# Performance work log

Hardware: AMD Instinct MI355X
Metric: run time of the kernel (lower is better)

## Reference

```python
import jax, jax.numpy as jnp
import numpy as np

NEG_INF = -9e15
ALPHA = 0.2  # LeakyReLU negative slope


def setup_inputs() -> dict:
    key = jax.random.key(0)
    k1, k2, k3, k4 = jax.random.split(key, 4)
    B, N, C_IN, C_OUT, H = 8, 2048, 256, 256, 4
    node_feats = jax.random.normal(k1, (B, N, C_IN), dtype=jnp.float32)
    adj_matrix = jax.random.randint(k2, (B, N, N), 0, 2, dtype=jnp.int32)
    # include self-connections as the docstring expects
    eye = jnp.eye(N, dtype=jnp.int32)[None]
    adj_matrix = jnp.maximum(adj_matrix, eye)
    W = jax.random.normal(k3, (C_OUT, C_IN), dtype=jnp.float32) * (1.414 / np.sqrt(C_IN))
    b = jnp.zeros((C_OUT,), dtype=jnp.float32)
    a = jax.random.normal(k4, (H, 2 * (C_OUT // H)), dtype=jnp.float32) * 0.1
    return {"node_feats": node_feats, "adj_matrix": adj_matrix, "W": W, "b": b, "a": a}


def reference(node_feats, adj_matrix, W, b, a):
    B, N, _ = node_feats.shape
    H, two_c = a.shape
    c = two_c // 2
    # projection: [B, N, H, c]
    f = (jnp.einsum('bni,oi->bno', node_feats, W) + b).reshape(B, N, H, c)
    # attention logit for edge (i, j): leakyrelu(a . [f_i, f_j])
    # decomposes as leakyrelu(s_src[i] + s_dst[j])
    a_src, a_dst = a[:, :c], a[:, c:]
    s_src = jnp.einsum('bnhc,hc->bnh', f, a_src)  # [B, N, H]
    s_dst = jnp.einsum('bnhc,hc->bnh', f, a_dst)  # [B, N, H]
    logits = jax.nn.leaky_relu(s_src[:, :, None, :] + s_dst[:, None, :, :], ALPHA)  # [B,N,N,H]
    logits = jnp.where(adj_matrix[..., None] == 1, logits, NEG_INF)
    probs = jax.nn.softmax(logits, axis=2)  # softmax over source nodes j
    out = jnp.einsum('bijh,bjhc->bihc', probs, f)
    return out.reshape(B, N, H * c)  # concat_heads=True
```

## Files before the change

### kernel.cpp

```cpp
#include <hip/hip_runtime.h>

#define LOG2E 1.4426950408889634f

typedef __attribute__((ext_vector_type(8))) short short8;
typedef __attribute__((ext_vector_type(16))) float f32x16;

__device__ __forceinline__ unsigned short f2bf(float f) {
  unsigned int u = __float_as_uint(f);
  u = (u + 0x7fffu + ((u >> 16) & 1u)) >> 16;
  return (unsigned short)u;
}

__global__ __launch_bounds__(256) void gat_k1(
    const float* __restrict__ X, const float* __restrict__ W,
    const float* __restrict__ bias, const float* __restrict__ a,
    unsigned short* __restrict__ ft, float* __restrict__ ssrc,
    float* __restrict__ sdst)
{
  __shared__ float Xs[8][128];
  __shared__ float Ws[8][128];
  const int tid = threadIdx.x;
  const int tx = tid & 15, ty = tid >> 4;
  const int m0 = blockIdx.x * 128;
  const int c0 = blockIdx.y * 128;

  float acc[8][8];
#pragma unroll
  for (int r = 0; r < 8; ++r)
#pragma unroll
    for (int j = 0; j < 8; ++j) acc[r][j] = 0.f;

  const int lrow = tid >> 1;
  const int kk0 = (tid & 1) * 4;
  const float* Xp = X + (size_t)(m0 + lrow) * 256 + kk0;
  const float* Wp = W + (size_t)(c0 + lrow) * 256 + kk0;

  for (int kc = 0; kc < 256; kc += 8) {
    float4 xv = *(const float4*)(Xp + kc);
    float4 wv = *(const float4*)(Wp + kc);
    __syncthreads();
    Xs[kk0 + 0][lrow] = xv.x; Xs[kk0 + 1][lrow] = xv.y;
    Xs[kk0 + 2][lrow] = xv.z; Xs[kk0 + 3][lrow] = xv.w;
    Ws[kk0 + 0][lrow] = wv.x; Ws[kk0 + 1][lrow] = wv.y;
    Ws[kk0 + 2][lrow] = wv.z; Ws[kk0 + 3][lrow] = wv.w;
    __syncthreads();
#pragma unroll
    for (int kk = 0; kk < 8; ++kk) {
      float av[8], wv8[8];
#pragma unroll
      for (int r = 0; r < 8; ++r) av[r] = Xs[kk][ty * 8 + r];
#pragma unroll
      for (int j = 0; j < 8; ++j) wv8[j] = Ws[kk][tx * 8 + j];
#pragma unroll
      for (int r = 0; r < 8; ++r)
#pragma unroll
        for (int j = 0; j < 8; ++j) acc[r][j] = fmaf(av[r], wv8[j], acc[r][j]);
    }
  }

  const int b = m0 >> 11;
  const int nloc0 = (m0 & 2047) + ty * 8;
  const int cg0 = c0 + tx * 8;
  const int h = cg0 >> 6;
  const int cb = cg0 & 63;

  float bv[8], av_s[8], av_d[8];
#pragma unroll
  for (int j = 0; j < 8; ++j) {
    bv[j]   = bias[cg0 + j];
    av_s[j] = a[h * 128 + cb + j];
    av_d[j] = a[h * 128 + 64 + cb + j];
  }
#pragma unroll
  for (int r = 0; r < 8; ++r)
#pragma unroll
    for (int j = 0; j < 8; ++j) acc[r][j] += bv[j];

  const int jt = nloc0 >> 4;
  const int ni = nloc0 & 15;
#pragma unroll
  for (int j = 0; j < 8; ++j) {
    unsigned int u[4];
#pragma unroll
    for (int q = 0; q < 4; ++q) {
      unsigned int lo = f2bf(acc[2 * q + 0][j]);
      unsigned int hi = f2bf(acc[2 * q + 1][j]);
      u[q] = lo | (hi << 16);
    }
    size_t off = ((((size_t)b * 128 + jt) * 4 + h) * 64 + (cb + j)) * 16 + ni;
    *(uint4*)(ft + off) = make_uint4(u[0], u[1], u[2], u[3]);
  }

  float sp[8], dp[8];
#pragma unroll
  for (int r = 0; r < 8; ++r) {
    float s = 0.f, d = 0.f;
#pragma unroll
    for (int j = 0; j < 8; ++j) {
      s = fmaf(acc[r][j], av_s[j], s);
      d = fmaf(acc[r][j], av_d[j], d);
    }
    sp[r] = s; dp[r] = d;
  }
#pragma unroll
  for (int off = 1; off < 8; off <<= 1) {
#pragma unroll
    for (int r = 0; r < 8; ++r) {
      sp[r] += __shfl_xor(sp[r], off);
      dp[r] += __shfl_xor(dp[r], off);
    }
  }
  if ((tx & 7) == 0) {
    float* sb = ssrc + ((size_t)b * 4 + h) * 2048 + nloc0;
    float* db = sdst + ((size_t)b * 4 + h) * 2048 + nloc0;
#pragma unroll
    for (int r = 0; r < 8; ++r) { sb[r] = sp[r] * LOG2E; db[r] = dp[r] * LOG2E; }
  }
}

__global__ __launch_bounds__(512, 4) void gat_k2(
    const int* __restrict__ adj, const unsigned short* __restrict__ ft,
    const float* __restrict__ ssrc, const float* __restrict__ sdst,
    float* __restrict__ out)
{
  __shared__ __align__(16) unsigned char lds[41216];
  float* sd = (float*)lds;
  unsigned* Aw = (unsigned*)(lds + 32768);

  const int tid = threadIdx.x;
  const int b = blockIdx.x & 7;
  const int itile = blockIdx.x >> 3;
  const int i0 = itile * 32;
  const int w = tid >> 6;
  const int h = w >> 1;
  const int p = w & 1;
  const int lane = tid & 63;
  const int l31 = lane & 31;
  const int kh = lane >> 5;
  const int shamt = (2 * p + kh) * 8;

  {
    const float4* src = (const float4*)(sdst + (size_t)b * 4 * 2048);
    float4* dst = (float4*)sd;
#pragma unroll
    for (int q = 0; q < 4; ++q) dst[tid + q * 512] = src[tid + q * 512];
  }
  {
    const int* abase = adj + (size_t)b * 2048 * 2048 + (size_t)i0 * 2048;
    unsigned short* dst16 = (unsigned short*)Aw;
#pragma unroll
    for (int k = 0; k < 8; ++k) {
      const int idx = k * 512 + tid;
      const int r = idx >> 7;
      const int s16 = idx & 127;
      const int4* ap = (const int4*)(abase + (size_t)r * 2048 + s16 * 16);
      int4 v0 = ap[0], v1 = ap[1], v2 = ap[2], v3 = ap[3];
      int vv[16] = {v0.x, v0.y, v0.z, v0.w, v1.x, v1.y, v1.z, v1.w,
                    v2.x, v2.y, v2.z, v2.w, v3.x, v3.y, v3.z, v3.w};
      unsigned m = 0;
#pragma unroll
      for (int i = 0; i < 16; ++i) m |= (vv[i] ? 1u : 0u) << i;
      dst16[(((s16 >> 1) * 33) + r) * 2 + (s16 & 1)] = (unsigned short)m;
    }
  }
  const float si = ssrc[((size_t)b * 4 + h) * 2048 + i0 + l31];

  const unsigned short* ftb =
      ft + ((((size_t)b * 128 + p) * 4 + h) * 64 + l31) * 16 + kh * 8;
  const float* sdh = sd + h * 2048 + p * 16 + kh * 8;

  f32x16 acc0, acc1;
#pragma unroll
  for (int q = 0; q < 16; ++q) { acc0[q] = 0.f; acc1[q] = 0.f; }
  float lsum = 0.f;

  __syncthreads();

  uint4 f0a, f0b, f1a, f1b, f2a, f2b, f3a, f3b;

#define LOADF(s, fa, fb)                                          \
  {                                                               \
    const unsigned short* fp_ = ftb + (size_t)(s) * 8192;         \
    fa = *(const uint4*)fp_;                                      \
    fb = *(const uint4*)(fp_ + 512);                              \
  }

#define COMP(s, fa, fb)                                           \
  {                                                               \
    const unsigned wrd = Aw[(s) * 33 + l31];                      \
    const unsigned byte_ = (wrd >> shamt) & 0xffu;                \
    const float* tp_ = sdh + (s) * 32;                            \
    float4 t0_ = *(const float4*)tp_;                             \
    float4 t1_ = *(const float4*)(tp_ + 4);                       \
    float tj_[8] = {t0_.x, t0_.y, t0_.z, t0_.w,                   \
                    t1_.x, t1_.y, t1_.z, t1_.w};                  \
    float e_[8];                                                  \
    _Pragma("unroll")                                             \
    for (int q = 0; q < 8; ++q) {                                 \
      float x_ = si + tj_[q];                                     \
      float y_ = fmaxf(x_, 0.2f * x_);                            \
      float ev_ = __builtin_amdgcn_exp2f(y_);                     \
      ev_ = (byte_ & (1u << q)) ? ev_ : 0.f;                      \
      e_[q] = ev_;                                                \
      lsum += ev_;                                                \
    }                                                             \
    union { unsigned u[4]; short8 v; } af_;                       \
    _Pragma("unroll")                                             \
    for (int q2 = 0; q2 < 4; ++q2) {                              \
      unsigned r_;                                                \
      asm("v_cvt_pk_bf16_f32 %0, %1, %2"                          \
          : "=v"(r_) : "v"(e_[2 * q2]), "v"(e_[2 * q2 + 1]));     \
      af_.u[q2] = r_;                                             \
    }                                                             \
    union { uint4 q; short8 v; } b0_, b1_;                        \
    b0_.q = fa; b1_.q = fb;                                       \
    acc0 = __builtin_amdgcn_mfma_f32_32x32x16_bf16(af_.v, b0_.v, acc0, 0, 0, 0); \
    acc1 = __builtin_amdgcn_mfma_f32_32x32x16_bf16(af_.v, b1_.v, acc1, 0, 0, 0); \
  }

  LOADF(0, f0a, f0b)
  LOADF(1, f1a, f1b)
  LOADF(2, f2a, f2b)
  LOADF(3, f3a, f3b)

  for (int s = 0; s < 64; s += 4) {
    const int n0 = (s + 4 < 64) ? s + 4 : 63;
    const int n1 = (s + 5 < 64) ? s + 5 : 63;
    const int n2 = (s + 6 < 64) ? s + 6 : 63;
    const int n3 = (s + 7 < 64) ? s + 7 : 63;
    COMP(s + 0, f0a, f0b) LOADF(n0, f0a, f0b)
    COMP(s + 1, f1a, f1b) LOADF(n1, f1a, f1b)
    COMP(s + 2, f2a, f2b) LOADF(n2, f2a, f2b)
    COMP(s + 3, f3a, f3b) LOADF(n3, f3a, f3b)
  }
#undef LOADF
#undef COMP

  float lsum2 = lsum + __shfl_xor(lsum, 32);
  float* ep = (float*)lds;
  float* el = (float*)(lds + 32768);
  __syncthreads();
  if (p == 1) {
#pragma unroll
    for (int reg = 0; reg < 16; ++reg) {
      const int row = (reg & 3) + 8 * (reg >> 2) + 4 * kh;
      ep[(h * 32 + row) * 64 + l31]      = acc0[reg];
      ep[(h * 32 + row) * 64 + l31 + 32] = acc1[reg];
    }
    if (lane < 32) el[h * 32 + l31] = lsum2;
  }
  __syncthreads();
  if (p == 0) {
    const float L = lsum2 + el[h * 32 + l31];
    const float rinv = 1.0f / L;
    float* ob = out + ((size_t)(b * 2048 + i0)) * 256 + h * 64;
#pragma unroll
    for (int reg = 0; reg < 16; ++reg) {
      const int row = (reg & 3) + 8 * (reg >> 2) + 4 * kh;
      const float ri = __shfl(rinv, row);
      const float o0 = (acc0[reg] + ep[(h * 32 + row) * 64 + l31]) * ri;
      const float o1 = (acc1[reg] + ep[(h * 32 + row) * 64 + l31 + 32]) * ri;
      ob[(size_t)row * 256 + l31]      = o0;
      ob[(size_t)row * 256 + l31 + 32] = o1;
    }
  }
}

extern "C" void kernel_launch(void* const* d_in, const int* in_sizes, int n_in,
                              void* d_out, int out_size, void* d_ws, size_t ws_size,
                              hipStream_t stream) {
  const float* X    = (const float*)d_in[0];
  const int*   adj  = (const int*)d_in[1];
  const float* W    = (const float*)d_in[2];
  const float* bias = (const float*)d_in[3];
  const float* a    = (const float*)d_in[4];
  float* out = (float*)d_out;

  unsigned short* ft = (unsigned short*)d_ws;
  float* ssrc = (float*)((char*)d_ws + 8388608);
  float* sdst = ssrc + 8 * 4 * 2048;

  gat_k1<<<dim3(128, 2, 1), 256, 0, stream>>>(X, W, bias, a, ft, ssrc, sdst);
  gat_k2<<<dim3(512, 1, 1), 512, 0, stream>>>(adj, ft, ssrc, sdst, out);
}
```

Baseline: 104.0 us.

## Halve row tile and switch to 16x16x32 MFMA for higher occupancy

```diff
diff --git a/kernel.cpp b/kernel.cpp
--- a/kernel.cpp
+++ b/kernel.cpp
@@ -3,7 +3,7 @@
 #define LOG2E 1.4426950408889634f
 
 typedef __attribute__((ext_vector_type(8))) short short8;
-typedef __attribute__((ext_vector_type(16))) float f32x16;
+typedef __attribute__((ext_vector_type(4))) float f32x4;
 
 __device__ __forceinline__ unsigned short f2bf(float f) {
   unsigned int u = __float_as_uint(f);
@@ -118,26 +118,26 @@
   }
 }
 
-__global__ __launch_bounds__(512, 4) void gat_k2(
+__global__ __launch_bounds__(512, 8) void gat_k2(
     const int* __restrict__ adj, const unsigned short* __restrict__ ft,
     const float* __restrict__ ssrc, const float* __restrict__ sdst,
     float* __restrict__ out)
 {
-  __shared__ __align__(16) unsigned char lds[41216];
+  __shared__ __align__(16) unsigned char lds[37120];
   float* sd = (float*)lds;
   unsigned* Aw = (unsigned*)(lds + 32768);
 
   const int tid = threadIdx.x;
   const int b = blockIdx.x & 7;
   const int itile = blockIdx.x >> 3;
-  const int i0 = itile * 32;
+  const int i0 = itile * 16;
   const int w = tid >> 6;
   const int h = w >> 1;
   const int p = w & 1;
   const int lane = tid & 63;
-  const int l31 = lane & 31;
-  const int kh = lane >> 5;
-  const int shamt = (2 * p + kh) * 8;
+  const int i_l = lane & 15;
+  const int kg = lane >> 4;
+  const int shamt = kg * 8;
 
   {
     const float4* src = (const float4*)(sdst + (size_t)b * 4 * 2048);
@@ -149,7 +149,7 @@
     const int* abase = adj + (size_t)b * 2048 * 2048 + (size_t)i0 * 2048;
     unsigned short* dst16 = (unsigned short*)Aw;
 #pragma unroll
-    for (int k = 0; k < 8; ++k) {
+    for (int k = 0; k < 4; ++k) {
       const int idx = k * 512 + tid;
       const int r = idx >> 7;
       const int s16 = idx & 127;
@@ -160,34 +160,25 @@
       unsigned m = 0;
 #pragma unroll
       for (int i = 0; i < 16; ++i) m |= (vv[i] ? 1u : 0u) << i;
-      dst16[(((s16 >> 1) * 33) + r) * 2 + (s16 & 1)] = (unsigned short)m;
-    }
-  }
-  const float si = ssrc[((size_t)b * 4 + h) * 2048 + i0 + l31];
-
+      dst16[((s16 >> 1) * 17 + r) * 2 + (s16 & 1)] = (unsigned short)m;
+    }
+  }
+  const float si = ssrc[((size_t)b * 4 + h) * 2048 + i0 + i_l];
+  const float* sdh = sd + h * 2048 + p * 1024 + kg * 8;
   const unsigned short* ftb =
-      ft + ((((size_t)b * 128 + p) * 4 + h) * 64 + l31) * 16 + kh * 8;
-  const float* sdh = sd + h * 2048 + p * 16 + kh * 8;
-
-  f32x16 acc0, acc1;
-#pragma unroll
-  for (int q = 0; q < 16; ++q) { acc0[q] = 0.f; acc1[q] = 0.f; }
+      ft + ((((size_t)b * 128 + p * 64 + (kg >> 1)) * 4 + h) * 64 + i_l) * 16 +
+      (kg & 1) * 8;
+
+  f32x4 acc0, acc1, acc2, acc3;
+#pragma unroll
+  for (int q = 0; q < 4; ++q) { acc0[q] = 0.f; acc1[q] = 0.f; acc2[q] = 0.f; acc3[q] = 0.f; }
   float lsum = 0.f;
 
   __syncthreads();
 
-  uint4 f0a, f0b, f1a, f1b, f2a, f2b, f3a, f3b;
-
-#define LOADF(s, fa, fb)                                          \
+#define COMP(s)                                                   \
   {                                                               \
-    const unsigned short* fp_ = ftb + (size_t)(s) * 8192;         \
-    fa = *(const uint4*)fp_;                                      \
-    fb = *(const uint4*)(fp_ + 512);                              \
-  }
-
-#define COMP(s, fa, fb)                                           \
-  {                                                               \
-    const unsigned wrd = Aw[(s) * 33 + l31];                      \
+    const unsigned wrd = Aw[(p * 32 + (s)) * 17 + i_l];           \
     const unsigned byte_ = (wrd >> shamt) & 0xffu;                \
     const float* tp_ = sdh + (s) * 32;                            \
     float4 t0_ = *(const float4*)tp_;                             \
@@ -212,56 +203,53 @@
           : "=v"(r_) : "v"(e_[2 * q2]), "v"(e_[2 * q2 + 1]));     \
       af_.u[q2] = r_;                                             \
     }                                                             \
-    union { uint4 q; short8 v; } b0_, b1_;                        \
-    b0_.q = fa; b1_.q = fb;                                       \
-    acc0 = __builtin_amdgcn_mfma_f32_32x32x16_bf16(af_.v, b0_.v, acc0, 0, 0, 0); \
-    acc1 = __builtin_amdgcn_mfma_f32_32x32x16_bf16(af_.v, b1_.v, acc1, 0, 0, 0); \
-  }
-
-  LOADF(0, f0a, f0b)
-  LOADF(1, f1a, f1b)
-  LOADF(2, f2a, f2b)
-  LOADF(3, f3a, f3b)
-
-  for (int s = 0; s < 64; s += 4) {
-    const int n0 = (s + 4 < 64) ? s + 4 : 63;
-    const int n1 = (s + 5 < 64) ? s + 5 : 63;
-    const int n2 = (s + 6 < 64) ? s + 6 : 63;
-    const int n3 = (s + 7 < 64) ? s + 7 : 63;
-    COMP(s + 0, f0a, f0b) LOADF(n0, f0a, f0b)
-    COMP(s + 1, f1a, f1b) LOADF(n1, f1a, f1b)
-    COMP(s + 2, f2a, f2b) LOADF(n2, f2a, f2b)
-    COMP(s + 3, f3a, f3b) LOADF(n3, f3a, f3b)
-  }
-#undef LOADF
+    const unsigned short* fp_ = ftb + (size_t)(s) * 8192;         \
+    union { uint4 q; short8 v; } b0_, b1_, b2_, b3_;              \
+    b0_.q = *(const uint4*)(fp_);                                 \
+    b1_.q = *(const uint4*)(fp_ + 256);                           \
+    b2_.q = *(const uint4*)(fp_ + 512);                           \
+    b3_.q = *(const uint4*)(fp_ + 768);                           \
+    acc0 = __builtin_amdgcn_mfma_f32_16x16x32_bf16(af_.v, b0_.v, acc0, 0, 0, 0); \
+    acc1 = __builtin_amdgcn_mfma_f32_16x16x32_bf16(af_.v, b1_.v, acc1, 0, 0, 0); \
+    acc2 = __builtin_amdgcn_mfma_f32_16x16x32_bf16(af_.v, b2_.v, acc2, 0, 0, 0); \
+    acc3 = __builtin_amdgcn_mfma_f32_16x16x32_bf16(af_.v, b3_.v, acc3, 0, 0, 0); \
+  }
+
+#pragma unroll 4
+  for (int s = 0; s < 32; ++s) {
+    COMP(s)
+  }
 #undef COMP
 
-  float lsum2 = lsum + __shfl_xor(lsum, 32);
+  float lsum2 = lsum + __shfl_xor(lsum, 16);
+  lsum2 += __shfl_xor(lsum2, 32);
   float* ep = (float*)lds;
-  float* el = (float*)(lds + 32768);
+  float* el = (float*)(lds + 16384);
   __syncthreads();
   if (p == 1) {
 #pragma unroll
-    for (int reg = 0; reg < 16; ++reg) {
-      const int row = (reg & 3) + 8 * (reg >> 2) + 4 * kh;
-      ep[(h * 32 + row) * 64 + l31]      = acc0[reg];
-      ep[(h * 32 + row) * 64 + l31 + 32] = acc1[reg];
-    }
-    if (lane < 32) el[h * 32 + l31] = lsum2;
+    for (int r = 0; r < 4; ++r) {
+      const int row = kg * 4 + r;
+      ep[(h * 16 + row) * 64 + 0  + i_l] = acc0[r];
+      ep[(h * 16 + row) * 64 + 16 + i_l] = acc1[r];
+      ep[(h * 16 + row) * 64 + 32 + i_l] = acc2[r];
+      ep[(h * 16 + row) * 64 + 48 + i_l] = acc3[r];
+    }
+    if (lane < 16) el[h * 16 + lane] = lsum2;
   }
   __syncthreads();
   if (p == 0) {
-    const float L = lsum2 + el[h * 32 + l31];
+    const float L = lsum2 + el[h * 16 + i_l];
     const float rinv = 1.0f / L;
     float* ob = out + ((size_t)(b * 2048 + i0)) * 256 + h * 64;
 #pragma unroll
-    for (int reg = 0; reg < 16; ++reg) {
-      const int row = (reg & 3) + 8 * (reg >> 2) + 4 * kh;
+    for (int r = 0; r < 4; ++r) {
+      const int row = kg * 4 + r;
       const float ri = __shfl(rinv, row);
-      const float o0 = (acc0[reg] + ep[(h * 32 + row) * 64 + l31]) * ri;
-      const float o1 = (acc1[reg] + ep[(h * 32 + row) * 64 + l31 + 32]) * ri;
-      ob[(size_t)row * 256 + l31]      = o0;
-      ob[(size_t)row * 256 + l31 + 32] = o1;
+      ob[(size_t)row * 256 + 0  + i_l] = (acc0[r] + ep[(h * 16 + row) * 64 + 0  + i_l]) * ri;
+      ob[(size_t)row * 256 + 16 + i_l] = (acc1[r] + ep[(h * 16 + row) * 64 + 16 + i_l]) * ri;
+      ob[(size_t)row * 256 + 32 + i_l] = (acc2[r] + ep[(h * 16 + row) * 64 + 32 + i_l]) * ri;
+      ob[(size_t)row * 256 + 48 + i_l] = (acc3[r] + ep[(h * 16 + row) * 64 + 48 + i_l]) * ri;
     }
   }
 }
@@ -281,5 +269,5 @@
   float* sdst = ssrc + 8 * 4 * 2048;
 
   gat_k1<<<dim3(128, 2, 1), 256, 0, stream>>>(X, W, bias, a, ft, ssrc, sdst);
-  gat_k2<<<dim3(512, 1, 1), 512, 0, stream>>>(adj, ft, ssrc, sdst, out);
-}
+  gat_k2<<<dim3(1024, 1, 1), 512, 0, stream>>>(adj, ft, ssrc, sdst, out);
+}
```

Measured after the change: 106.5 us. 2.4% more time.
